# Kernel optimization log

Hardware: AMD Instinct MI355X
Metric: run time of the kernel (lower is better)

Reference implementation:

```python
import jax, jax.numpy as jnp
import numpy as np

N, X_DIM, Y_DIM, HID = 1024, 256, 256, 256  # HID = hidden_size // 2


def setup_inputs() -> dict:
    key = jax.random.key(0)
    ks = jax.random.split(key, 11)
    s_in = 1.0 / np.sqrt(X_DIM)
    s_h = 1.0 / np.sqrt(HID)
    return {
        "x_samples": jax.random.normal(ks[0], (N, X_DIM), jnp.float32),
        "y_samples": jax.random.normal(ks[1], (N, Y_DIM), jnp.float32),
        "z_samples": jax.random.normal(ks[2], (N, Y_DIM), jnp.float32),
        "w1_mu": jax.random.uniform(ks[3], (HID, X_DIM), jnp.float32, -s_in, s_in),
        "b1_mu": jax.random.uniform(ks[4], (HID,), jnp.float32, -s_in, s_in),
        "w2_mu": jax.random.uniform(ks[5], (Y_DIM, HID), jnp.float32, -s_h, s_h),
        "b2_mu": jax.random.uniform(ks[6], (Y_DIM,), jnp.float32, -s_h, s_h),
        "w1_lv": jax.random.uniform(ks[7], (HID, X_DIM), jnp.float32, -s_in, s_in),
        "b1_lv": jax.random.uniform(ks[8], (HID,), jnp.float32, -s_in, s_in),
        "w2_lv": jax.random.uniform(ks[9], (Y_DIM, HID), jnp.float32, -s_h, s_h),
        "b2_lv": jax.random.uniform(ks[10], (Y_DIM,), jnp.float32, -s_h, s_h),
    }


def reference(x_samples, y_samples, z_samples,
              w1_mu, b1_mu, w2_mu, b2_mu,
              w1_lv, b1_lv, w2_lv, b2_lv):
    # MLP heads (torch Linear: x @ W.T + b)
    h_mu = jax.nn.relu(x_samples @ w1_mu.T + b1_mu)
    mu = h_mu @ w2_mu.T + b2_mu                       # [N, D]
    h_lv = jax.nn.relu(x_samples @ w1_lv.T + b1_lv)
    logvar = jnp.tanh(h_lv @ w2_lv.T + b2_lv)          # [N, D]

    inv2var = 1.0 / (2.0 * jnp.exp(logvar))           # [N, D]

    # positive: per-sample conditional log-density term
    positive = -((mu - y_samples) ** 2 + (mu - z_samples) ** 2) * inv2var  # [N, D]

    # negative: mean over all pairings (i: prediction, j: sample)
    # pairwise squared diffs materialize [N, N, D] like the original broadcast
    pred = mu[:, None, :]                              # [N, 1, D]
    sq = (y_samples[None, :, :] - pred) ** 2 + (z_samples[None, :, :] - pred) ** 2
    negative = -sq.mean(axis=1) * inv2var              # [N, D]

    return jax.nn.relu(positive.sum(axis=-1) - negative.sum(axis=-1)).mean()
```

## Files before the change

### kernel.cpp

```cpp
#include <hip/hip_runtime.h>
#include <math.h>

constexpr int KT = 64;
constexpr int LSB = 72;

typedef short bf16x8 __attribute__((ext_vector_type(8)));
typedef float f32x4  __attribute__((ext_vector_type(4)));

__device__ __forceinline__ unsigned short f2bf_rne(float f) {
    unsigned u = __float_as_uint(f);
    unsigned r = (u + 0x7fff + ((u >> 16) & 1)) >> 16;
    return (unsigned short)r;
}
__device__ __forceinline__ float bf2f(unsigned short h) {
    return __uint_as_float(((unsigned)h) << 16);
}

template <bool SUMRELU_A>
__device__ __forceinline__ void gemm_tile_mfma(const float* __restrict__ A0,
                                               const float* __restrict__ A1,
                                               const float* __restrict__ B,
                                               const float* __restrict__ bias,
                                               float* __restrict__ C,
                                               int rowBase, int colBase, int k0) {
    const int t = threadIdx.x;
    const int w    = t >> 6;
    const int lane = t & 63;
    const int quad = lane >> 4;
    const int mr   = lane & 15;

    __shared__ __align__(16) unsigned short Ah[64][LSB];
    __shared__ __align__(16) unsigned short Al[64][LSB];
    __shared__ __align__(16) unsigned short Bh[64][LSB];
    __shared__ __align__(16) unsigned short Bl[64][LSB];

    f32x4 acc[4] = {{0.f, 0.f, 0.f, 0.f}, {0.f, 0.f, 0.f, 0.f},
                    {0.f, 0.f, 0.f, 0.f}, {0.f, 0.f, 0.f, 0.f}};

    for (int kt = k0; kt < k0 + 128; kt += KT) {
#pragma unroll
        for (int p = 0; p < 4; p++) {
            int idx = p * 256 + t;
            int r = idx >> 4;
            int k4 = idx & 15;
            int off = (rowBase + r) * 256 + kt + k4 * 4;
            float4 av = *(const float4*)&A0[off];
            if (SUMRELU_A) {
                float4 a1 = *(const float4*)&A1[off];
                av.x = fmaxf(av.x + a1.x, 0.f);
                av.y = fmaxf(av.y + a1.y, 0.f);
                av.z = fmaxf(av.z + a1.z, 0.f);
                av.w = fmaxf(av.w + a1.w, 0.f);
            }
            float4 bv = *(const float4*)&B[(colBase + r) * 256 + kt + k4 * 4];

            ushort4 ahv, alv, bhv, blv;
            ahv.x = f2bf_rne(av.x); alv.x = f2bf_rne(av.x - bf2f(ahv.x));
            ahv.y = f2bf_rne(av.y); alv.y = f2bf_rne(av.y - bf2f(ahv.y));
            ahv.z = f2bf_rne(av.z); alv.z = f2bf_rne(av.z - bf2f(ahv.z));
            ahv.w = f2bf_rne(av.w); alv.w = f2bf_rne(av.w - bf2f(ahv.w));
            bhv.x = f2bf_rne(bv.x); blv.x = f2bf_rne(bv.x - bf2f(bhv.x));
            bhv.y = f2bf_rne(bv.y); blv.y = f2bf_rne(bv.y - bf2f(bhv.y));
            bhv.z = f2bf_rne(bv.z); blv.z = f2bf_rne(bv.z - bf2f(bhv.z));
            bhv.w = f2bf_rne(bv.w); blv.w = f2bf_rne(bv.w - bf2f(bhv.w));

            *(ushort4*)&Ah[r][k4 * 4] = ahv;
            *(ushort4*)&Al[r][k4 * 4] = alv;
            *(ushort4*)&Bh[r][k4 * 4] = bhv;
            *(ushort4*)&Bl[r][k4 * 4] = blv;
        }
        __syncthreads();

#pragma unroll
        for (int kk = 0; kk < KT; kk += 32) {
            int ko = kk + quad * 8;
            bf16x8 ah = *(const bf16x8*)&Ah[w * 16 + mr][ko];
            bf16x8 al = *(const bf16x8*)&Al[w * 16 + mr][ko];
#pragma unroll
            for (int c = 0; c < 4; c++) {
                bf16x8 bh = *(const bf16x8*)&Bh[c * 16 + mr][ko];
                bf16x8 bl = *(const bf16x8*)&Bl[c * 16 + mr][ko];
                acc[c] = __builtin_amdgcn_mfma_f32_16x16x32_bf16(ah, bh, acc[c], 0, 0, 0);
                acc[c] = __builtin_amdgcn_mfma_f32_16x16x32_bf16(ah, bl, acc[c], 0, 0, 0);
                acc[c] = __builtin_amdgcn_mfma_f32_16x16x32_bf16(al, bh, acc[c], 0, 0, 0);
            }
        }
        __syncthreads();
    }

    float bcol[4] = {0.f, 0.f, 0.f, 0.f};
    if (bias) {
#pragma unroll
        for (int c = 0; c < 4; c++) bcol[c] = bias[colBase + c * 16 + mr];
    }
#pragma unroll
    for (int c = 0; c < 4; c++) {
#pragma unroll
        for (int reg = 0; reg < 4; reg++) {
            int rg = rowBase + w * 16 + quad * 4 + reg;
            int cg = colBase + c * 16 + mr;
            C[rg * 256 + cg] = acc[c][reg] + bcol[c];
        }
    }
}

#define DECODE_GEMM(bid, chunk, head, rowBase, colBase, k0) \
    int chunk = (bid) & 1;                                  \
    int head  = ((bid) >> 1) & 1;                           \
    int colBase = (((bid) >> 2) & 3) * 64;                  \
    int rowBase = ((bid) >> 4) * 64;                        \
    int k0 = chunk * 128;

__global__ __launch_bounds__(256)
void k1_layer1(const float* __restrict__ x,
               const float* __restrict__ w1m, const float* __restrict__ w1l,
               const float* __restrict__ b1m, const float* __restrict__ b1l,
               float* __restrict__ hm0, float* __restrict__ hm1,
               float* __restrict__ hl0, float* __restrict__ hl1,
               const float* __restrict__ y, const float* __restrict__ z,
               float* __restrict__ pA1, float* __restrict__ pB1,
               float* __restrict__ out) {
    int bid = blockIdx.x;
    int t = threadIdx.x;
    DECODE_GEMM(bid, chunk, head, rowBase, colBase, k0)
    const float* Bw = head ? w1l : w1m;
    const float* bias = chunk ? nullptr : (head ? b1l : b1m);
    float* C = head ? (chunk ? hl1 : hl0) : (chunk ? hm1 : hm0);
    gemm_tile_mfma<false>(x, nullptr, Bw, bias, C, rowBase, colBase, k0);

    float sA = 0.f, sB = 0.f;
    int base = bid * 4 * 256 + t;
#pragma unroll
    for (int j = 0; j < 4; j++) {
        float yv = y[base + j * 256];
        float zv = z[base + j * 256];
        sA += yv * yv + zv * zv;
        sB += yv + zv;
    }
    pA1[bid * 256 + t] = sA;
    pB1[bid * 256 + t] = sB;
    if (bid == 0 && t == 0) out[0] = 0.f;
}

__global__ __launch_bounds__(256)
void k2_layer2(const float* __restrict__ hm0, const float* __restrict__ hm1,
               const float* __restrict__ hl0, const float* __restrict__ hl1,
               const float* __restrict__ w2m, const float* __restrict__ w2l,
               const float* __restrict__ b2m, const float* __restrict__ b2l,
               float* __restrict__ mu0, float* __restrict__ mu1,
               float* __restrict__ lv0, float* __restrict__ lv1,
               const float* __restrict__ pA1, const float* __restrict__ pB1,
               float* __restrict__ pA2, float* __restrict__ pB2) {
    int bid = blockIdx.x;
    int t = threadIdx.x;
    DECODE_GEMM(bid, chunk, head, rowBase, colBase, k0)
    const float* A0 = head ? hl0 : hm0;
    const float* A1 = head ? hl1 : hm1;
    const float* Bw = head ? w2l : w2m;
    const float* bias = chunk ? nullptr : (head ? b2l : b2m);
    float* C = head ? (chunk ? lv1 : lv0) : (chunk ? mu1 : mu0);
    gemm_tile_mfma<true>(A0, A1, Bw, bias, C, rowBase, colBase, k0);

    if (bid < 16) {
        float sA = 0.f, sB = 0.f;
#pragma unroll
        for (int s = 0; s < 16; s++) {
            int o = (bid * 16 + s) * 256 + t;
            sA += pA1[o];
            sB += pB1[o];
        }
        pA2[bid * 256 + t] = sA;
        pB2[bid * 256 + t] = sB;
    }
}

__global__ __launch_bounds__(256)
void k3_epilogue(const float* __restrict__ mu0, const float* __restrict__ mu1,
                 const float* __restrict__ lv0, const float* __restrict__ lv1,
                 const float* __restrict__ y, const float* __restrict__ z,
                 const float* __restrict__ pA2, const float* __restrict__ pB2,
                 float* __restrict__ out) {
    __shared__ float red[4];
    int t = threadIdx.x;
    int lane = t & 63, wave = t >> 6;

    float mA = 0.f, mB = 0.f;
#pragma unroll
    for (int g = 0; g < 16; g++) {
        mA += pA2[g * 256 + t];
        mB += pB2[g * 256 + t];
    }
    mA *= (1.f / 1024.f);
    mB *= (1.f / 1024.f);

    float blockSum = 0.f;
    for (int r = 0; r < 4; r++) {
        int o = (blockIdx.x * 4 + r) * 256 + t;
        float m  = mu0[o] + mu1[o];
        float lv = tanhf(lv0[o] + lv1[o]);
        float iv = 0.5f * expf(-lv);
        float yv = y[o];
        float zv = z[o];
        float Mt = mA - 2.f * m * mB + 2.f * m * m;
        float dy = m - yv, dz = m - zv;
        float term = iv * (Mt - dy * dy - dz * dz);
#pragma unroll
        for (int mask = 32; mask; mask >>= 1)
            term += __shfl_xor(term, mask, 64);
        if (lane == 0) red[wave] = term;
        __syncthreads();
        if (t == 0) {
            float rs = red[0] + red[1] + red[2] + red[3];
            blockSum += fmaxf(rs, 0.f);
        }
        __syncthreads();
    }
    if (t == 0) atomicAdd(out, blockSum * (1.f / 1024.f));
}

extern "C" void kernel_launch(void* const* d_in, const int* in_sizes, int n_in,
                              void* d_out, int out_size, void* d_ws, size_t ws_size,
                              hipStream_t stream) {
    const float* x   = (const float*)d_in[0];
    const float* y   = (const float*)d_in[1];
    const float* zs  = (const float*)d_in[2];
    const float* w1m = (const float*)d_in[3];
    const float* b1m = (const float*)d_in[4];
    const float* w2m = (const float*)d_in[5];
    const float* b2m = (const float*)d_in[6];
    const float* w1l = (const float*)d_in[7];
    const float* b1l = (const float*)d_in[8];
    const float* w2l = (const float*)d_in[9];
    const float* b2l = (const float*)d_in[10];
    float* out = (float*)d_out;

    char* ws = (char*)d_ws;
    float* pA2 = (float*)(ws);
    float* pB2 = (float*)(ws + (16u << 10));
    float* pA1 = (float*)(ws + (256u << 10));
    float* pB1 = (float*)(ws + (512u << 10));
    float* buf = (float*)(ws + (1u << 20));
    const unsigned MB = (1u << 20) / 4;
    float* hm0 = buf + 0 * MB;
    float* hm1 = buf + 1 * MB;
    float* hl0 = buf + 2 * MB;
    float* hl1 = buf + 3 * MB;
    float* mu0 = buf + 4 * MB;
    float* mu1 = buf + 5 * MB;
    float* lv0 = buf + 6 * MB;
    float* lv1 = buf + 7 * MB;

    k1_layer1<<<256, 256, 0, stream>>>(x, w1m, w1l, b1m, b1l,
                                       hm0, hm1, hl0, hl1,
                                       y, zs, pA1, pB1, out);
    k2_layer2<<<256, 256, 0, stream>>>(hm0, hm1, hl0, hl1,
                                       w2m, w2l, b2m, b2l,
                                       mu0, mu1, lv0, lv1,
                                       pA1, pB1, pA2, pB2);
    k3_epilogue<<<256, 256, 0, stream>>>(mu0, mu1, lv0, lv1,
                                         y, zs, pA2, pB2, out);
}
```

Measured before the change: 102.0 us.

## Fuse layer-2 GEMM with loss epilogue using atomic row accumulation and tickets

Merges the second-layer GEMM and the epilogue into one kernel. Each block now computes full-K 32x32 tiles for both the mu and logvar heads together and evaluates the loss terms directly from shared memory, so the mu/logvar partial buffers are no longer written to and read back from global memory. Per-row sums are accumulated with atomics, and a per-row-tile ticket counter lets the last block apply the ReLU and add to the output. This removes one kernel launch and the intermediate traffic, at the cost of smaller tiles, redundant column-sum reductions in every block, and atomic contention.

```diff
diff --git a/kernel.cpp b/kernel.cpp
--- a/kernel.cpp
+++ b/kernel.cpp
@@ -15,10 +15,14 @@
 __device__ __forceinline__ float bf2f(unsigned short h) {
     return __uint_as_float(((unsigned)h) << 16);
 }
-
-template <bool SUMRELU_A>
+__device__ __forceinline__ void split4(float4 v, ushort4& hi, ushort4& lo) {
+    hi.x = f2bf_rne(v.x); lo.x = f2bf_rne(v.x - bf2f(hi.x));
+    hi.y = f2bf_rne(v.y); lo.y = f2bf_rne(v.y - bf2f(hi.y));
+    hi.z = f2bf_rne(v.z); lo.z = f2bf_rne(v.z - bf2f(hi.z));
+    hi.w = f2bf_rne(v.w); lo.w = f2bf_rne(v.w - bf2f(hi.w));
+}
+
 __device__ __forceinline__ void gemm_tile_mfma(const float* __restrict__ A0,
-                                               const float* __restrict__ A1,
                                                const float* __restrict__ B,
                                                const float* __restrict__ bias,
                                                float* __restrict__ C,
@@ -43,31 +47,15 @@
             int idx = p * 256 + t;
             int r = idx >> 4;
             int k4 = idx & 15;
-            int off = (rowBase + r) * 256 + kt + k4 * 4;
-            float4 av = *(const float4*)&A0[off];
-            if (SUMRELU_A) {
-                float4 a1 = *(const float4*)&A1[off];
-                av.x = fmaxf(av.x + a1.x, 0.f);
-                av.y = fmaxf(av.y + a1.y, 0.f);
-                av.z = fmaxf(av.z + a1.z, 0.f);
-                av.w = fmaxf(av.w + a1.w, 0.f);
-            }
+            float4 av = *(const float4*)&A0[(rowBase + r) * 256 + kt + k4 * 4];
             float4 bv = *(const float4*)&B[(colBase + r) * 256 + kt + k4 * 4];
-
-            ushort4 ahv, alv, bhv, blv;
-            ahv.x = f2bf_rne(av.x); alv.x = f2bf_rne(av.x - bf2f(ahv.x));
-            ahv.y = f2bf_rne(av.y); alv.y = f2bf_rne(av.y - bf2f(ahv.y));
-            ahv.z = f2bf_rne(av.z); alv.z = f2bf_rne(av.z - bf2f(ahv.z));
-            ahv.w = f2bf_rne(av.w); alv.w = f2bf_rne(av.w - bf2f(ahv.w));
-            bhv.x = f2bf_rne(bv.x); blv.x = f2bf_rne(bv.x - bf2f(bhv.x));
-            bhv.y = f2bf_rne(bv.y); blv.y = f2bf_rne(bv.y - bf2f(bhv.y));
-            bhv.z = f2bf_rne(bv.z); blv.z = f2bf_rne(bv.z - bf2f(bhv.z));
-            bhv.w = f2bf_rne(bv.w); blv.w = f2bf_rne(bv.w - bf2f(bhv.w));
-
-            *(ushort4*)&Ah[r][k4 * 4] = ahv;
-            *(ushort4*)&Al[r][k4 * 4] = alv;
-            *(ushort4*)&Bh[r][k4 * 4] = bhv;
-            *(ushort4*)&Bl[r][k4 * 4] = blv;
+            ushort4 h4, l4;
+            split4(av, h4, l4);
+            *(ushort4*)&Ah[r][k4 * 4] = h4;
+            *(ushort4*)&Al[r][k4 * 4] = l4;
+            split4(bv, h4, l4);
+            *(ushort4*)&Bh[r][k4 * 4] = h4;
+            *(ushort4*)&Bl[r][k4 * 4] = l4;
         }
         __syncthreads();
 
@@ -103,13 +91,6 @@
         }
     }
 }
-
-#define DECODE_GEMM(bid, chunk, head, rowBase, colBase, k0) \
-    int chunk = (bid) & 1;                                  \
-    int head  = ((bid) >> 1) & 1;                           \
-    int colBase = (((bid) >> 2) & 3) * 64;                  \
-    int rowBase = ((bid) >> 4) * 64;                        \
-    int k0 = chunk * 128;
 
 __global__ __launch_bounds__(256)
 void k1_layer1(const float* __restrict__ x,
@@ -119,14 +100,19 @@
                float* __restrict__ hl0, float* __restrict__ hl1,
                const float* __restrict__ y, const float* __restrict__ z,
                float* __restrict__ pA1, float* __restrict__ pB1,
+               float* __restrict__ rowAcc, int* __restrict__ tick,
                float* __restrict__ out) {
     int bid = blockIdx.x;
     int t = threadIdx.x;
-    DECODE_GEMM(bid, chunk, head, rowBase, colBase, k0)
+    int chunk = bid & 1;
+    int head  = (bid >> 1) & 1;
+    int colBase = ((bid >> 2) & 3) * 64;
+    int rowBase = (bid >> 4) * 64;
+    int k0 = chunk * 128;
     const float* Bw = head ? w1l : w1m;
     const float* bias = chunk ? nullptr : (head ? b1l : b1m);
     float* C = head ? (chunk ? hl1 : hl0) : (chunk ? hm1 : hm0);
-    gemm_tile_mfma<false>(x, nullptr, Bw, bias, C, rowBase, colBase, k0);
+    gemm_tile_mfma(x, Bw, bias, C, rowBase, colBase, k0);
 
     float sA = 0.f, sB = 0.f;
     int base = bid * 4 * 256 + t;
@@ -139,83 +125,168 @@
     }
     pA1[bid * 256 + t] = sA;
     pB1[bid * 256 + t] = sB;
+
+    if (bid < 4) rowAcc[bid * 256 + t] = 0.f;
+    if (bid == 4 && t < 32) tick[t] = 0;
     if (bid == 0 && t == 0) out[0] = 0.f;
 }
 
 __global__ __launch_bounds__(256)
-void k2_layer2(const float* __restrict__ hm0, const float* __restrict__ hm1,
-               const float* __restrict__ hl0, const float* __restrict__ hl1,
-               const float* __restrict__ w2m, const float* __restrict__ w2l,
-               const float* __restrict__ b2m, const float* __restrict__ b2l,
-               float* __restrict__ mu0, float* __restrict__ mu1,
-               float* __restrict__ lv0, float* __restrict__ lv1,
-               const float* __restrict__ pA1, const float* __restrict__ pB1,
-               float* __restrict__ pA2, float* __restrict__ pB2) {
-    int bid = blockIdx.x;
-    int t = threadIdx.x;
-    DECODE_GEMM(bid, chunk, head, rowBase, colBase, k0)
-    const float* A0 = head ? hl0 : hm0;
-    const float* A1 = head ? hl1 : hm1;
-    const float* Bw = head ? w2l : w2m;
-    const float* bias = chunk ? nullptr : (head ? b2l : b2m);
-    float* C = head ? (chunk ? lv1 : lv0) : (chunk ? mu1 : mu0);
-    gemm_tile_mfma<true>(A0, A1, Bw, bias, C, rowBase, colBase, k0);
-
-    if (bid < 16) {
+void k2_fused(const float* __restrict__ hm0, const float* __restrict__ hm1,
+              const float* __restrict__ hl0, const float* __restrict__ hl1,
+              const float* __restrict__ w2m, const float* __restrict__ w2l,
+              const float* __restrict__ b2m, const float* __restrict__ b2l,
+              const float* __restrict__ y, const float* __restrict__ z,
+              const float* __restrict__ pA1, const float* __restrict__ pB1,
+              float* __restrict__ rowAcc, int* __restrict__ tick,
+              float* __restrict__ out) {
+    const int bid = blockIdx.x;
+    const int t = threadIdx.x;
+    const int rt = bid >> 3;
+    const int ct = bid & 7;
+    const int w = t >> 6, lane = t & 63, quad = lane >> 4, mr = lane & 15;
+    const int h = w & 1, mt = w >> 1;
+
+    __shared__ __align__(16) unsigned short Apl[2][2][32][LSB];
+    __shared__ __align__(16) unsigned short Bpl[2][2][32][LSB];
+    __shared__ float Cx[2][32][33];
+    __shared__ float part[16][32];
+    __shared__ float mAf[32], mBf[32];
+
+    {
+        int c = t & 31, g8 = t >> 5;
+        int gc = ct * 32 + c;
         float sA = 0.f, sB = 0.f;
-#pragma unroll
-        for (int s = 0; s < 16; s++) {
-            int o = (bid * 16 + s) * 256 + t;
-            sA += pA1[o];
-            sB += pB1[o];
-        }
-        pA2[bid * 256 + t] = sA;
-        pB2[bid * 256 + t] = sB;
-    }
-}
-
-__global__ __launch_bounds__(256)
-void k3_epilogue(const float* __restrict__ mu0, const float* __restrict__ mu1,
-                 const float* __restrict__ lv0, const float* __restrict__ lv1,
-                 const float* __restrict__ y, const float* __restrict__ z,
-                 const float* __restrict__ pA2, const float* __restrict__ pB2,
-                 float* __restrict__ out) {
-    __shared__ float red[4];
-    int t = threadIdx.x;
-    int lane = t & 63, wave = t >> 6;
-
-    float mA = 0.f, mB = 0.f;
-#pragma unroll
-    for (int g = 0; g < 16; g++) {
-        mA += pA2[g * 256 + t];
-        mB += pB2[g * 256 + t];
-    }
-    mA *= (1.f / 1024.f);
-    mB *= (1.f / 1024.f);
-
-    float blockSum = 0.f;
-    for (int r = 0; r < 4; r++) {
-        int o = (blockIdx.x * 4 + r) * 256 + t;
-        float m  = mu0[o] + mu1[o];
-        float lv = tanhf(lv0[o] + lv1[o]);
-        float iv = 0.5f * expf(-lv);
-        float yv = y[o];
-        float zv = z[o];
-        float Mt = mA - 2.f * m * mB + 2.f * m * m;
-        float dy = m - yv, dz = m - zv;
-        float term = iv * (Mt - dy * dy - dz * dz);
-#pragma unroll
-        for (int mask = 32; mask; mask >>= 1)
-            term += __shfl_xor(term, mask, 64);
-        if (lane == 0) red[wave] = term;
+        for (int j = 0; j < 32; j++) {
+            int s = g8 * 32 + j;
+            sA += pA1[s * 256 + gc];
+            sB += pB1[s * 256 + gc];
+        }
+        part[g8][c] = sA;
+        part[8 + g8][c] = sB;
+    }
+    __syncthreads();
+    if (t < 32) {
+        float sA = 0.f, sB = 0.f;
+#pragma unroll
+        for (int g = 0; g < 8; g++) { sA += part[g][t]; sB += part[8 + g][t]; }
+        mAf[t] = sA * (1.f / 1024.f);
+        mBf[t] = sB * (1.f / 1024.f);
+    }
+
+    f32x4 acc[2] = {{0.f, 0.f, 0.f, 0.f}, {0.f, 0.f, 0.f, 0.f}};
+
+    for (int kt = 0; kt < 256; kt += KT) {
+#pragma unroll
+        for (int p = 0; p < 2; p++) {
+            int idx = p * 256 + t;
+            int r = idx >> 4;
+            int k4 = idx & 15;
+            int off  = (rt * 32 + r) * 256 + kt + k4 * 4;
+            int boff = (ct * 32 + r) * 256 + kt + k4 * 4;
+            float4 m0 = *(const float4*)&hm0[off];
+            float4 m1 = *(const float4*)&hm1[off];
+            float4 l0 = *(const float4*)&hl0[off];
+            float4 l1 = *(const float4*)&hl1[off];
+            float4 am, av;
+            am.x = fmaxf(m0.x + m1.x, 0.f); am.y = fmaxf(m0.y + m1.y, 0.f);
+            am.z = fmaxf(m0.z + m1.z, 0.f); am.w = fmaxf(m0.w + m1.w, 0.f);
+            av.x = fmaxf(l0.x + l1.x, 0.f); av.y = fmaxf(l0.y + l1.y, 0.f);
+            av.z = fmaxf(l0.z + l1.z, 0.f); av.w = fmaxf(l0.w + l1.w, 0.f);
+            float4 bm = *(const float4*)&w2m[boff];
+            float4 bv = *(const float4*)&w2l[boff];
+            ushort4 h4, l4;
+            split4(am, h4, l4);
+            *(ushort4*)&Apl[0][0][r][k4 * 4] = h4;
+            *(ushort4*)&Apl[0][1][r][k4 * 4] = l4;
+            split4(av, h4, l4);
+            *(ushort4*)&Apl[1][0][r][k4 * 4] = h4;
+            *(ushort4*)&Apl[1][1][r][k4 * 4] = l4;
+            split4(bm, h4, l4);
+            *(ushort4*)&Bpl[0][0][r][k4 * 4] = h4;
+            *(ushort4*)&Bpl[0][1][r][k4 * 4] = l4;
+            split4(bv, h4, l4);
+            *(ushort4*)&Bpl[1][0][r][k4 * 4] = h4;
+            *(ushort4*)&Bpl[1][1][r][k4 * 4] = l4;
+        }
         __syncthreads();
-        if (t == 0) {
-            float rs = red[0] + red[1] + red[2] + red[3];
-            blockSum += fmaxf(rs, 0.f);
+
+#pragma unroll
+        for (int kk = 0; kk < KT; kk += 32) {
+            int ko = kk + quad * 8;
+            bf16x8 ah = *(const bf16x8*)&Apl[h][0][mt * 16 + mr][ko];
+            bf16x8 al = *(const bf16x8*)&Apl[h][1][mt * 16 + mr][ko];
+#pragma unroll
+            for (int nt = 0; nt < 2; nt++) {
+                bf16x8 bh = *(const bf16x8*)&Bpl[h][0][nt * 16 + mr][ko];
+                bf16x8 bl = *(const bf16x8*)&Bpl[h][1][nt * 16 + mr][ko];
+                acc[nt] = __builtin_amdgcn_mfma_f32_16x16x32_bf16(ah, bh, acc[nt], 0, 0, 0);
+                acc[nt] = __builtin_amdgcn_mfma_f32_16x16x32_bf16(ah, bl, acc[nt], 0, 0, 0);
+                acc[nt] = __builtin_amdgcn_mfma_f32_16x16x32_bf16(al, bh, acc[nt], 0, 0, 0);
+            }
         }
         __syncthreads();
     }
-    if (t == 0) atomicAdd(out, blockSum * (1.f / 1024.f));
+
+    {
+        const float* b2 = h ? b2l : b2m;
+#pragma unroll
+        for (int nt = 0; nt < 2; nt++) {
+            int cl = nt * 16 + mr;
+            float bb = b2[ct * 32 + cl];
+#pragma unroll
+            for (int reg = 0; reg < 4; reg++) {
+                int rl = mt * 16 + quad * 4 + reg;
+                Cx[h][rl][cl] = acc[nt][reg] + bb;
+            }
+        }
+    }
+    __syncthreads();
+
+    {
+        int half = lane >> 5;
+        int col = lane & 31;
+        int gcol = ct * 32 + col;
+        float mA = mAf[col], mB = mBf[col];
+#pragma unroll
+        for (int sub = 0; sub < 4; sub++) {
+            int row = w * 8 + sub * 2 + half;
+            int grow = rt * 32 + row;
+            float m = Cx[0][row][col];
+            float lv = tanhf(Cx[1][row][col]);
+            float iv = 0.5f * expf(-lv);
+            float yv = y[grow * 256 + gcol];
+            float zv = z[grow * 256 + gcol];
+            float Mt = mA - 2.f * m * mB + 2.f * m * m;
+            float dy = m - yv, dz = m - zv;
+            float term = iv * (Mt - dy * dy - dz * dz);
+#pragma unroll
+            for (int msk = 16; msk; msk >>= 1)
+                term += __shfl_xor(term, msk, 32);
+            if (col == 0) atomicAdd(&rowAcc[grow], term);
+        }
+    }
+
+    __threadfence();
+    __syncthreads();
+
+    if (w == 0) {
+        int old = 0;
+        if (lane == 0) old = atomicAdd(&tick[rt], 1);
+        old = __shfl(old, 0, 64);
+        if (old == 7) {
+            __threadfence();
+            float v = 0.f;
+            if (lane < 32)
+                v = fmaxf(__hip_atomic_load(&rowAcc[rt * 32 + lane],
+                                            __ATOMIC_RELAXED,
+                                            __HIP_MEMORY_SCOPE_AGENT), 0.f);
+#pragma unroll
+            for (int msk = 16; msk; msk >>= 1)
+                v += __shfl_xor(v, msk, 32);
+            if (lane == 0) atomicAdd(out, v * (1.f / 1024.f));
+        }
+    }
 }
 
 extern "C" void kernel_launch(void* const* d_in, const int* in_sizes, int n_in,
@@ -235,28 +306,21 @@
     float* out = (float*)d_out;
 
     char* ws = (char*)d_ws;
-    float* pA2 = (float*)(ws);
-    float* pB2 = (float*)(ws + (16u << 10));
-    float* pA1 = (float*)(ws + (256u << 10));
-    float* pB1 = (float*)(ws + (512u << 10));
-    float* buf = (float*)(ws + (1u << 20));
+    float* pA1    = (float*)(ws);
+    float* pB1    = (float*)(ws + (256u << 10));
+    float* rowAcc = (float*)(ws + (512u << 10));
+    int*   tick   = (int*)(ws + (520u << 10));
+    float* buf    = (float*)(ws + (1u << 20));
     const unsigned MB = (1u << 20) / 4;
     float* hm0 = buf + 0 * MB;
     float* hm1 = buf + 1 * MB;
     float* hl0 = buf + 2 * MB;
     float* hl1 = buf + 3 * MB;
-    float* mu0 = buf + 4 * MB;
-    float* mu1 = buf + 5 * MB;
-    float* lv0 = buf + 6 * MB;
-    float* lv1 = buf + 7 * MB;
 
     k1_layer1<<<256, 256, 0, stream>>>(x, w1m, w1l, b1m, b1l,
                                        hm0, hm1, hl0, hl1,
-                                       y, zs, pA1, pB1, out);
-    k2_layer2<<<256, 256, 0, stream>>>(hm0, hm1, hl0, hl1,
-                                       w2m, w2l, b2m, b2l,
-                                       mu0, mu1, lv0, lv1,
-                                       pA1, pB1, pA2, pB2);
-    k3_epilogue<<<256, 256, 0, stream>>>(mu0, mu1, lv0, lv1,
-                                         y, zs, pA2, pB2, out);
-}
+                                       y, zs, pA1, pB1, rowAcc, tick, out);
+    k2_fused<<<256, 256, 0, stream>>>(hm0, hm1, hl0, hl1,
+                                      w2m, w2l, b2m, b2l,
+                                      y, zs, pA1, pB1, rowAcc, tick, out);
+}
```

New measurement: 112.5 us. +10.3%, slower.

## Replace split-K with full-K 64x32 tiles and pre-split bf16 intermediates

Applied to the files above, without the earlier changes.

The GEMM tiling moves from split-K 64x64 tiles with two partial outputs to full-K 64x32 tiles, so the partial-sum buffers and their re-summing in later kernels go away. Layer 1 now applies bias and ReLU in its epilogue and writes the hidden activations as pre-split bf16 hi/lo halves. It also pre-splits the layer-2 weights, so layer 2 only copies bf16 data into shared memory instead of converting fp32. This cuts intermediate global traffic and conversion work, at the cost of a longer K loop per block and smaller N tiles that reuse A less.

```diff
diff --git a/kernel.cpp b/kernel.cpp
--- a/kernel.cpp
+++ b/kernel.cpp
@@ -1,7 +1,6 @@
 #include <hip/hip_runtime.h>
 #include <math.h>
 
-constexpr int KT = 64;
 constexpr int LSB = 72;
 
 typedef short bf16x8 __attribute__((ext_vector_type(8)));
@@ -15,151 +14,185 @@
 __device__ __forceinline__ float bf2f(unsigned short h) {
     return __uint_as_float(((unsigned)h) << 16);
 }
-
-template <bool SUMRELU_A>
-__device__ __forceinline__ void gemm_tile_mfma(const float* __restrict__ A0,
-                                               const float* __restrict__ A1,
-                                               const float* __restrict__ B,
-                                               const float* __restrict__ bias,
-                                               float* __restrict__ C,
-                                               int rowBase, int colBase, int k0) {
-    const int t = threadIdx.x;
-    const int w    = t >> 6;
-    const int lane = t & 63;
-    const int quad = lane >> 4;
-    const int mr   = lane & 15;
-
-    __shared__ __align__(16) unsigned short Ah[64][LSB];
-    __shared__ __align__(16) unsigned short Al[64][LSB];
-    __shared__ __align__(16) unsigned short Bh[64][LSB];
-    __shared__ __align__(16) unsigned short Bl[64][LSB];
-
-    f32x4 acc[4] = {{0.f, 0.f, 0.f, 0.f}, {0.f, 0.f, 0.f, 0.f},
-                    {0.f, 0.f, 0.f, 0.f}, {0.f, 0.f, 0.f, 0.f}};
-
-    for (int kt = k0; kt < k0 + 128; kt += KT) {
-#pragma unroll
-        for (int p = 0; p < 4; p++) {
-            int idx = p * 256 + t;
-            int r = idx >> 4;
-            int k4 = idx & 15;
-            int off = (rowBase + r) * 256 + kt + k4 * 4;
-            float4 av = *(const float4*)&A0[off];
-            if (SUMRELU_A) {
-                float4 a1 = *(const float4*)&A1[off];
-                av.x = fmaxf(av.x + a1.x, 0.f);
-                av.y = fmaxf(av.y + a1.y, 0.f);
-                av.z = fmaxf(av.z + a1.z, 0.f);
-                av.w = fmaxf(av.w + a1.w, 0.f);
-            }
-            float4 bv = *(const float4*)&B[(colBase + r) * 256 + kt + k4 * 4];
-
-            ushort4 ahv, alv, bhv, blv;
-            ahv.x = f2bf_rne(av.x); alv.x = f2bf_rne(av.x - bf2f(ahv.x));
-            ahv.y = f2bf_rne(av.y); alv.y = f2bf_rne(av.y - bf2f(ahv.y));
-            ahv.z = f2bf_rne(av.z); alv.z = f2bf_rne(av.z - bf2f(ahv.z));
-            ahv.w = f2bf_rne(av.w); alv.w = f2bf_rne(av.w - bf2f(ahv.w));
-            bhv.x = f2bf_rne(bv.x); blv.x = f2bf_rne(bv.x - bf2f(bhv.x));
-            bhv.y = f2bf_rne(bv.y); blv.y = f2bf_rne(bv.y - bf2f(bhv.y));
-            bhv.z = f2bf_rne(bv.z); blv.z = f2bf_rne(bv.z - bf2f(bhv.z));
-            bhv.w = f2bf_rne(bv.w); blv.w = f2bf_rne(bv.w - bf2f(bhv.w));
-
-            *(ushort4*)&Ah[r][k4 * 4] = ahv;
-            *(ushort4*)&Al[r][k4 * 4] = alv;
-            *(ushort4*)&Bh[r][k4 * 4] = bhv;
-            *(ushort4*)&Bl[r][k4 * 4] = blv;
-        }
-        __syncthreads();
-
-#pragma unroll
-        for (int kk = 0; kk < KT; kk += 32) {
-            int ko = kk + quad * 8;
-            bf16x8 ah = *(const bf16x8*)&Ah[w * 16 + mr][ko];
-            bf16x8 al = *(const bf16x8*)&Al[w * 16 + mr][ko];
-#pragma unroll
-            for (int c = 0; c < 4; c++) {
-                bf16x8 bh = *(const bf16x8*)&Bh[c * 16 + mr][ko];
-                bf16x8 bl = *(const bf16x8*)&Bl[c * 16 + mr][ko];
-                acc[c] = __builtin_amdgcn_mfma_f32_16x16x32_bf16(ah, bh, acc[c], 0, 0, 0);
-                acc[c] = __builtin_amdgcn_mfma_f32_16x16x32_bf16(ah, bl, acc[c], 0, 0, 0);
-                acc[c] = __builtin_amdgcn_mfma_f32_16x16x32_bf16(al, bh, acc[c], 0, 0, 0);
-            }
-        }
-        __syncthreads();
-    }
-
-    float bcol[4] = {0.f, 0.f, 0.f, 0.f};
-    if (bias) {
-#pragma unroll
-        for (int c = 0; c < 4; c++) bcol[c] = bias[colBase + c * 16 + mr];
-    }
-#pragma unroll
-    for (int c = 0; c < 4; c++) {
-#pragma unroll
-        for (int reg = 0; reg < 4; reg++) {
-            int rg = rowBase + w * 16 + quad * 4 + reg;
-            int cg = colBase + c * 16 + mr;
-            C[rg * 256 + cg] = acc[c][reg] + bcol[c];
-        }
-    }
-}
-
-#define DECODE_GEMM(bid, chunk, head, rowBase, colBase, k0) \
-    int chunk = (bid) & 1;                                  \
-    int head  = ((bid) >> 1) & 1;                           \
-    int colBase = (((bid) >> 2) & 3) * 64;                  \
-    int rowBase = ((bid) >> 4) * 64;                        \
-    int k0 = chunk * 128;
+__device__ __forceinline__ void split4(float4 v, ushort4& hi, ushort4& lo) {
+    hi.x = f2bf_rne(v.x); lo.x = f2bf_rne(v.x - bf2f(hi.x));
+    hi.y = f2bf_rne(v.y); lo.y = f2bf_rne(v.y - bf2f(hi.y));
+    hi.z = f2bf_rne(v.z); lo.z = f2bf_rne(v.z - bf2f(hi.z));
+    hi.w = f2bf_rne(v.w); lo.w = f2bf_rne(v.w - bf2f(hi.w));
+}
+
 
 __global__ __launch_bounds__(256)
 void k1_layer1(const float* __restrict__ x,
                const float* __restrict__ w1m, const float* __restrict__ w1l,
                const float* __restrict__ b1m, const float* __restrict__ b1l,
-               float* __restrict__ hm0, float* __restrict__ hm1,
-               float* __restrict__ hl0, float* __restrict__ hl1,
+               const float* __restrict__ w2m, const float* __restrict__ w2l,
+               unsigned short* __restrict__ hmH, unsigned short* __restrict__ hmL,
+               unsigned short* __restrict__ hlH, unsigned short* __restrict__ hlL,
+               unsigned short* __restrict__ w2mH, unsigned short* __restrict__ w2mL,
+               unsigned short* __restrict__ w2lH, unsigned short* __restrict__ w2lL,
                const float* __restrict__ y, const float* __restrict__ z,
                float* __restrict__ pA1, float* __restrict__ pB1,
                float* __restrict__ out) {
-    int bid = blockIdx.x;
-    int t = threadIdx.x;
-    DECODE_GEMM(bid, chunk, head, rowBase, colBase, k0)
-    const float* Bw = head ? w1l : w1m;
-    const float* bias = chunk ? nullptr : (head ? b1l : b1m);
-    float* C = head ? (chunk ? hl1 : hl0) : (chunk ? hm1 : hm0);
-    gemm_tile_mfma<false>(x, nullptr, Bw, bias, C, rowBase, colBase, k0);
-
-    float sA = 0.f, sB = 0.f;
-    int base = bid * 4 * 256 + t;
-#pragma unroll
-    for (int j = 0; j < 4; j++) {
-        float yv = y[base + j * 256];
-        float zv = z[base + j * 256];
-        sA += yv * yv + zv * zv;
-        sB += yv + zv;
-    }
-    pA1[bid * 256 + t] = sA;
-    pB1[bid * 256 + t] = sB;
+    const int bid = blockIdx.x, t = threadIdx.x;
+    const int head = bid & 1, ct = (bid >> 1) & 7, rt = bid >> 4;
+    const int rowBase = rt * 64, colBase = ct * 32;
+    const int w = t >> 6, lane = t & 63, quad = lane >> 4, mr = lane & 15;
+
+    const float* Bw   = head ? w1l : w1m;
+    const float* bias = head ? b1l : b1m;
+    unsigned short* CH = head ? hlH : hmH;
+    unsigned short* CL = head ? hlL : hmL;
+
+    __shared__ __align__(16) unsigned short Ah[64][LSB], Al[64][LSB];
+    __shared__ __align__(16) unsigned short Bh[32][LSB], Bl[32][LSB];
+
+    f32x4 acc[2] = {{0.f, 0.f, 0.f, 0.f}, {0.f, 0.f, 0.f, 0.f}};
+
+    for (int kt = 0; kt < 256; kt += 64) {
+#pragma unroll
+        for (int p = 0; p < 4; p++) {
+            int idx = p * 256 + t;
+            int r = idx >> 4, k4 = idx & 15;
+            float4 av = *(const float4*)&x[(rowBase + r) * 256 + kt + k4 * 4];
+            ushort4 h4, l4;
+            split4(av, h4, l4);
+            *(ushort4*)&Ah[r][k4 * 4] = h4;
+            *(ushort4*)&Al[r][k4 * 4] = l4;
+            if (p < 2) {
+                float4 bv = *(const float4*)&Bw[(colBase + r) * 256 + kt + k4 * 4];
+                split4(bv, h4, l4);
+                *(ushort4*)&Bh[r][k4 * 4] = h4;
+                *(ushort4*)&Bl[r][k4 * 4] = l4;
+            }
+        }
+        __syncthreads();
+
+#pragma unroll
+        for (int kk = 0; kk < 64; kk += 32) {
+            int ko = kk + quad * 8;
+            bf16x8 ah = *(const bf16x8*)&Ah[w * 16 + mr][ko];
+            bf16x8 al = *(const bf16x8*)&Al[w * 16 + mr][ko];
+#pragma unroll
+            for (int nt = 0; nt < 2; nt++) {
+                bf16x8 bh = *(const bf16x8*)&Bh[nt * 16 + mr][ko];
+                bf16x8 bl = *(const bf16x8*)&Bl[nt * 16 + mr][ko];
+                acc[nt] = __builtin_amdgcn_mfma_f32_16x16x32_bf16(ah, bh, acc[nt], 0, 0, 0);
+                acc[nt] = __builtin_amdgcn_mfma_f32_16x16x32_bf16(ah, bl, acc[nt], 0, 0, 0);
+                acc[nt] = __builtin_amdgcn_mfma_f32_16x16x32_bf16(al, bh, acc[nt], 0, 0, 0);
+            }
+        }
+        __syncthreads();
+    }
+
+#pragma unroll
+    for (int nt = 0; nt < 2; nt++) {
+        int cg = colBase + nt * 16 + mr;
+        float bb = bias[cg];
+#pragma unroll
+        for (int reg = 0; reg < 4; reg++) {
+            int rg = rowBase + w * 16 + quad * 4 + reg;
+            float v = fmaxf(acc[nt][reg] + bb, 0.f);
+            unsigned short hi = f2bf_rne(v);
+            CH[rg * 256 + cg] = hi;
+            CL[rg * 256 + cg] = f2bf_rne(v - bf2f(hi));
+        }
+    }
+
+    {
+        int off = bid * 256 + t;
+        float vm = w2m[off], vl = w2l[off];
+        unsigned short h1 = f2bf_rne(vm);
+        w2mH[off] = h1; w2mL[off] = f2bf_rne(vm - bf2f(h1));
+        unsigned short h2 = f2bf_rne(vl);
+        w2lH[off] = h2; w2lL[off] = f2bf_rne(vl - bf2f(h2));
+    }
+
+    {
+        float sA = 0.f, sB = 0.f;
+        int base = bid * 4 * 256 + t;
+#pragma unroll
+        for (int j = 0; j < 4; j++) {
+            float yv = y[base + j * 256];
+            float zv = z[base + j * 256];
+            sA += yv * yv + zv * zv;
+            sB += yv + zv;
+        }
+        pA1[bid * 256 + t] = sA;
+        pB1[bid * 256 + t] = sB;
+    }
     if (bid == 0 && t == 0) out[0] = 0.f;
 }
 
 __global__ __launch_bounds__(256)
-void k2_layer2(const float* __restrict__ hm0, const float* __restrict__ hm1,
-               const float* __restrict__ hl0, const float* __restrict__ hl1,
-               const float* __restrict__ w2m, const float* __restrict__ w2l,
+void k2_layer2(const unsigned short* __restrict__ hmH, const unsigned short* __restrict__ hmL,
+               const unsigned short* __restrict__ hlH, const unsigned short* __restrict__ hlL,
+               const unsigned short* __restrict__ w2mH, const unsigned short* __restrict__ w2mL,
+               const unsigned short* __restrict__ w2lH, const unsigned short* __restrict__ w2lL,
                const float* __restrict__ b2m, const float* __restrict__ b2l,
-               float* __restrict__ mu0, float* __restrict__ mu1,
-               float* __restrict__ lv0, float* __restrict__ lv1,
+               float* __restrict__ muO, float* __restrict__ lvO,
                const float* __restrict__ pA1, const float* __restrict__ pB1,
                float* __restrict__ pA2, float* __restrict__ pB2) {
-    int bid = blockIdx.x;
-    int t = threadIdx.x;
-    DECODE_GEMM(bid, chunk, head, rowBase, colBase, k0)
-    const float* A0 = head ? hl0 : hm0;
-    const float* A1 = head ? hl1 : hm1;
-    const float* Bw = head ? w2l : w2m;
-    const float* bias = chunk ? nullptr : (head ? b2l : b2m);
-    float* C = head ? (chunk ? lv1 : lv0) : (chunk ? mu1 : mu0);
-    gemm_tile_mfma<true>(A0, A1, Bw, bias, C, rowBase, colBase, k0);
+    const int bid = blockIdx.x, t = threadIdx.x;
+    const int head = bid & 1, ct = (bid >> 1) & 7, rt = bid >> 4;
+    const int rowBase = rt * 64, colBase = ct * 32;
+    const int w = t >> 6, lane = t & 63, quad = lane >> 4, mr = lane & 15;
+
+    const unsigned short* AH = head ? hlH : hmH;
+    const unsigned short* AL = head ? hlL : hmL;
+    const unsigned short* BH = head ? w2lH : w2mH;
+    const unsigned short* BL = head ? w2lL : w2mL;
+    const float* bias = head ? b2l : b2m;
+    float* C = head ? lvO : muO;
+
+    __shared__ __align__(16) unsigned short Ah[64][LSB], Al[64][LSB];
+    __shared__ __align__(16) unsigned short Bh[32][LSB], Bl[32][LSB];
+
+    f32x4 acc[2] = {{0.f, 0.f, 0.f, 0.f}, {0.f, 0.f, 0.f, 0.f}};
+
+    for (int kt = 0; kt < 256; kt += 64) {
+#pragma unroll
+        for (int p = 0; p < 4; p++) {
+            int idx = p * 256 + t;
+            int r = idx >> 4, k4 = idx & 15;
+            int off = (rowBase + r) * 256 + kt + k4 * 4;
+            *(ushort4*)&Ah[r][k4 * 4] = *(const ushort4*)&AH[off];
+            *(ushort4*)&Al[r][k4 * 4] = *(const ushort4*)&AL[off];
+            if (p < 2) {
+                int boff = (colBase + r) * 256 + kt + k4 * 4;
+                *(ushort4*)&Bh[r][k4 * 4] = *(const ushort4*)&BH[boff];
+                *(ushort4*)&Bl[r][k4 * 4] = *(const ushort4*)&BL[boff];
+            }
+        }
+        __syncthreads();
+
+#pragma unroll
+        for (int kk = 0; kk < 64; kk += 32) {
+            int ko = kk + quad * 8;
+            bf16x8 ah = *(const bf16x8*)&Ah[w * 16 + mr][ko];
+            bf16x8 al = *(const bf16x8*)&Al[w * 16 + mr][ko];
+#pragma unroll
+            for (int nt = 0; nt < 2; nt++) {
+                bf16x8 bh = *(const bf16x8*)&Bh[nt * 16 + mr][ko];
+                bf16x8 bl = *(const bf16x8*)&Bl[nt * 16 + mr][ko];
+                acc[nt] = __builtin_amdgcn_mfma_f32_16x16x32_bf16(ah, bh, acc[nt], 0, 0, 0);
+                acc[nt] = __builtin_amdgcn_mfma_f32_16x16x32_bf16(ah, bl, acc[nt], 0, 0, 0);
+                acc[nt] = __builtin_amdgcn_mfma_f32_16x16x32_bf16(al, bh, acc[nt], 0, 0, 0);
+            }
+        }
+        __syncthreads();
+    }
+
+#pragma unroll
+    for (int nt = 0; nt < 2; nt++) {
+        int cg = colBase + nt * 16 + mr;
+        float bb = bias[cg];
+#pragma unroll
+        for (int reg = 0; reg < 4; reg++) {
+            int rg = rowBase + w * 16 + quad * 4 + reg;
+            C[rg * 256 + cg] = acc[nt][reg] + bb;
+        }
+    }
 
     if (bid < 16) {
         float sA = 0.f, sB = 0.f;
@@ -175,8 +208,7 @@
 }
 
 __global__ __launch_bounds__(256)
-void k3_epilogue(const float* __restrict__ mu0, const float* __restrict__ mu1,
-                 const float* __restrict__ lv0, const float* __restrict__ lv1,
+void k3_epilogue(const float* __restrict__ muO, const float* __restrict__ lvO,
                  const float* __restrict__ y, const float* __restrict__ z,
                  const float* __restrict__ pA2, const float* __restrict__ pB2,
                  float* __restrict__ out) {
@@ -196,8 +228,8 @@
     float blockSum = 0.f;
     for (int r = 0; r < 4; r++) {
         int o = (blockIdx.x * 4 + r) * 256 + t;
-        float m  = mu0[o] + mu1[o];
-        float lv = tanhf(lv0[o] + lv1[o]);
+        float m  = muO[o];
+        float lv = tanhf(lvO[o]);
         float iv = 0.5f * expf(-lv);
         float yv = y[o];
         float zv = z[o];
@@ -235,28 +267,28 @@
     float* out = (float*)d_out;
 
     char* ws = (char*)d_ws;
-    float* pA2 = (float*)(ws);
-    float* pB2 = (float*)(ws + (16u << 10));
-    float* pA1 = (float*)(ws + (256u << 10));
-    float* pB1 = (float*)(ws + (512u << 10));
-    float* buf = (float*)(ws + (1u << 20));
-    const unsigned MB = (1u << 20) / 4;
-    float* hm0 = buf + 0 * MB;
-    float* hm1 = buf + 1 * MB;
-    float* hl0 = buf + 2 * MB;
-    float* hl1 = buf + 3 * MB;
-    float* mu0 = buf + 4 * MB;
-    float* mu1 = buf + 5 * MB;
-    float* lv0 = buf + 6 * MB;
-    float* lv1 = buf + 7 * MB;
-
-    k1_layer1<<<256, 256, 0, stream>>>(x, w1m, w1l, b1m, b1l,
-                                       hm0, hm1, hl0, hl1,
+    float* pA1 = (float*)(ws);
+    float* pB1 = (float*)(ws + (256u << 10));
+    float* pA2 = (float*)(ws + (512u << 10));
+    float* pB2 = (float*)(ws + (528u << 10));
+    unsigned short* hmH = (unsigned short*)(ws + (1024u << 10));
+    unsigned short* hmL = (unsigned short*)(ws + (1536u << 10));
+    unsigned short* hlH = (unsigned short*)(ws + (2048u << 10));
+    unsigned short* hlL = (unsigned short*)(ws + (2560u << 10));
+    unsigned short* w2mH = (unsigned short*)(ws + (3072u << 10));
+    unsigned short* w2mL = (unsigned short*)(ws + (3200u << 10));
+    unsigned short* w2lH = (unsigned short*)(ws + (3328u << 10));
+    unsigned short* w2lL = (unsigned short*)(ws + (3456u << 10));
+    float* muO = (float*)(ws + (4096u << 10));
+    float* lvO = (float*)(ws + (5120u << 10));
+
+    k1_layer1<<<256, 256, 0, stream>>>(x, w1m, w1l, b1m, b1l, w2m, w2l,
+                                       hmH, hmL, hlH, hlL,
+                                       w2mH, w2mL, w2lH, w2lL,
                                        y, zs, pA1, pB1, out);
-    k2_layer2<<<256, 256, 0, stream>>>(hm0, hm1, hl0, hl1,
-                                       w2m, w2l, b2m, b2l,
-                                       mu0, mu1, lv0, lv1,
+    k2_layer2<<<256, 256, 0, stream>>>(hmH, hmL, hlH, hlL,
+                                       w2mH, w2mL, w2lH, w2lL,
+                                       b2m, b2l, muO, lvO,
                                        pA1, pB1, pA2, pB2);
-    k3_epilogue<<<256, 256, 0, stream>>>(mu0, mu1, lv0, lv1,
-                                         y, zs, pA2, pB2, out);
-}
+    k3_epilogue<<<256, 256, 0, stream>>>(muO, lvO, y, zs, pA2, pB2, out);
+}
```

Result: no change. 100.5 us (-1.5%).
